# Kernel optimization log

Measured on AMD Instinct MI355X. Metric: run time of the kernel, lower is better.

Reference implementation:

```python
import jax, jax.numpy as jnp
import numpy as np

C, H, W = 8, 8, 8
A = 6            # action_dim
LATENT = 64
HID = 64
GRU_IN = HID + A + LATENT  # 134


def _conv(x, w):
    return jax.lax.conv_general_dilated(
        x, w, (1, 1), 'VALID', dimension_numbers=('NCHW', 'OIHW', 'NCHW'))


def setup_inputs() -> dict:
    key = jax.random.key(0)
    ks = jax.random.split(key, 20)
    B, N, T = 64, 10, 128
    s_h = jax.random.normal(ks[0], (B, N, T, C, H, W), jnp.float32)
    a_h = jax.random.randint(ks[1], (B, N, T), 0, A).astype(jnp.int64)
    b_z = jax.random.normal(ks[2], (B, LATENT), jnp.float32)
    s = 0.05
    p = {
        'conv1_w': jax.random.normal(ks[3], (32, C, 3, 3)) * s,
        'conv1_b': jnp.zeros((32,)),
        'conv2_w': jax.random.normal(ks[4], (32, 32, 3, 3)) * s,
        'conv2_b': jnp.zeros((32,)),
        'fc_w': jax.random.normal(ks[5], (HID, 32 * 4 * 4)) * s,
        'fc_b': jnp.zeros((HID,)),
        'emb': jax.random.normal(ks[6], (A, A)) * s,
        'gru_wih': jax.random.normal(ks[7], (3 * HID, GRU_IN)) * s,
        'gru_whh': jax.random.normal(ks[8], (3 * HID, HID)) * s,
        'gru_bih': jnp.zeros((3 * HID,)),
        'gru_bhh': jnp.zeros((3 * HID,)),
        'mlp1_w': jax.random.normal(ks[9], (HID, HID)) * s,
        'mlp1_b': jnp.zeros((HID,)),
        'mlp2_w': jax.random.normal(ks[10], (A, HID)) * s,
        'mlp2_b': jnp.zeros((A,)),
    }
    return {'s_h': s_h, 'a_h': a_h, 'b_z': b_z, **p}


def reference(s_h, a_h, b_z, conv1_w, conv1_b, conv2_w, conv2_b, fc_w, fc_b,
              emb, gru_wih, gru_whh, gru_bih, gru_bhh,
              mlp1_w, mlp1_b, mlp2_w, mlp2_b):
    B, N = s_h.shape[0], s_h.shape[1]
    T = a_h.shape[2]
    BN = B * N

    # action mask, [B, N, T, 1]
    action_masks = (a_h != A - 1)[..., None].astype(jnp.float32)

    # --- state encoder on first frame only ---
    s0 = s_h[:, :, 0].reshape(BN, C, H, W)
    x = jax.nn.relu(_conv(s0, conv1_w) + conv1_b[:, None, None])
    x = jax.nn.relu(_conv(x, conv2_w) + conv2_b[:, None, None])
    x = x.reshape(BN, -1)                       # [BN, 512]
    state_emb = jax.nn.relu(x @ fc_w.T + fc_b)  # [BN, HID]

    bz = jnp.broadcast_to(b_z[:, None, :], (B, N, LATENT)).reshape(BN, LATENT)

    h0 = jnp.zeros((BN, HID), s_h.dtype)
    act0 = jnp.full((BN,), A - 1, jnp.int32)

    def step(carry, _):
        h, act = carry
        a_emb = emb[act]                                          # [BN, A]
        inp = jnp.concatenate([state_emb, a_emb, bz], axis=-1)    # [BN, GRU_IN]
        gx = inp @ gru_wih.T + gru_bih
        gh = h @ gru_whh.T + gru_bhh
        xr, xz, xn = jnp.split(gx, 3, axis=-1)
        hr, hz, hn = jnp.split(gh, 3, axis=-1)
        r = jax.nn.sigmoid(xr + hr)
        z = jax.nn.sigmoid(xz + hz)
        n = jnp.tanh(xn + r * hn)
        h_new = (1.0 - z) * n + z * h
        hid = jnp.tanh(h_new @ mlp1_w.T + mlp1_b)
        logits = hid @ mlp2_w.T + mlp2_b                          # [BN, A]
        next_act = jax.lax.stop_gradient(jnp.argmax(logits, axis=-1)).astype(jnp.int32)
        return (h_new, next_act), logits

    (_, _), logits_seq = jax.lax.scan(step, (h0, act0), None, length=T - 1)
    # logits_seq: [T-1, BN, A] -> [B, N, T-1, A]
    logits_all = jnp.transpose(logits_seq, (1, 0, 2)).reshape(B, N, T - 1, A)
    return logits_all, action_masks
```

## Files before the change

kernel.cpp:

```cpp
#include <hip/hip_runtime.h>

#define A_DIM 6
#define HID_D 64
#define LATENT_D 64
#define GRU_IN_D 134
#define T_STEPS 128
#define N_ENV 10
#define BN_TOT 640

typedef float f2 __attribute__((ext_vector_type(2)));

__device__ __forceinline__ float fast_sigmoid(float x) {
    return __builtin_amdgcn_rcpf(1.0f + __builtin_amdgcn_exp2f(-1.4426950408889634f * x));
}
__device__ __forceinline__ float fast_tanh(float x) {
    return 1.0f - 2.0f * __builtin_amdgcn_rcpf(1.0f + __builtin_amdgcn_exp2f(2.8853900817779268f * x));
}

template<int CTRL>
__device__ __forceinline__ float dppadd(float v) {
    int t = __builtin_amdgcn_update_dpp(0, __builtin_bit_cast(int, v), CTRL, 0xf, 0xf, true);
    return v + __builtin_bit_cast(float, t);
}
__device__ __forceinline__ float wave_reduce_add(float v) {
    v = dppadd<0x111>(v);
    v = dppadd<0x112>(v);
    v = dppadd<0x114>(v);
    v = dppadd<0x118>(v);
    v = dppadd<0x142>(v);
    v = dppadd<0x143>(v);
    return __builtin_bit_cast(float, __builtin_amdgcn_readlane(__builtin_bit_cast(int, v), 63));
}

__global__ __launch_bounds__(128, 1)
void policy_kernel(const float* __restrict__ s_h,
                   const int*   __restrict__ a_h,
                   const float* __restrict__ b_z,
                   const float* __restrict__ conv1_w, const float* __restrict__ conv1_b,
                   const float* __restrict__ conv2_w, const float* __restrict__ conv2_b,
                   const float* __restrict__ fc_w,    const float* __restrict__ fc_b,
                   const float* __restrict__ emb,
                   const float* __restrict__ gru_wih, const float* __restrict__ gru_whh,
                   const float* __restrict__ gru_bih, const float* __restrict__ gru_bhh,
                   const float* __restrict__ mlp1_w,  const float* __restrict__ mlp1_b,
                   const float* __restrict__ mlp2_w,  const float* __restrict__ mlp2_b,
                   float* __restrict__ logits_out, float* __restrict__ mask_out)
{
    __shared__ __align__(16) float s0[512];
    __shared__ __align__(16) float a1[1152];
    __shared__ __align__(16) float a2[512];
    __shared__ __align__(16) float pfc[128];
    __shared__ __align__(16) float semb[64];
    __shared__ __align__(16) float gxc[192];
    __shared__ __align__(16) float atab[6*192];
    __shared__ __align__(16) float hspec[6*64];
    __shared__ f2 lwn2[2048];
    __shared__ f2 lw12[2048];

    const int bn  = blockIdx.x;
    const int tid = threadIdx.x;
    const int j   = tid & 63;
    const int w   = tid >> 6;

    mask_out[bn * T_STEPS + tid] = (a_h[bn * T_STEPS + tid] != (A_DIM - 1)) ? 1.0f : 0.0f;

    {
        const float* src = s_h + (size_t)bn * T_STEPS * 512;
        #pragma unroll
        for (int i = 0; i < 4; ++i) s0[tid + i * 128] = src[tid + i * 128];
    }

    for (int i2 = tid; i2 < 2048; i2 += 128) {
        const int k2 = i2 >> 6, jj = i2 & 63;
        lwn2[i2] = *(const f2*)&gru_whh[(128 + jj) * 64 + 2 * k2];
        lw12[i2] = *(const f2*)&mlp1_w[(size_t)jj * 64 + 2 * k2];
    }
    __syncthreads();

    for (int i = tid; i < 1152; i += 128) {
        const int oc = i / 36, r = i % 36, oh = r / 6, ow = r % 6;
        float sum = conv1_b[oc];
        const float* wp = conv1_w + oc * 72;
        #pragma unroll
        for (int ic = 0; ic < 8; ++ic)
            #pragma unroll
            for (int kh = 0; kh < 3; ++kh)
                #pragma unroll
                for (int kw = 0; kw < 3; ++kw)
                    sum = fmaf(s0[ic * 64 + (oh + kh) * 8 + (ow + kw)],
                               wp[ic * 9 + kh * 3 + kw], sum);
        a1[i] = fmaxf(sum, 0.0f);
    }
    __syncthreads();

    for (int i = tid; i < 512; i += 128) {
        const int oc = i / 16, r = i % 16, oh = r / 4, ow = r % 4;
        float sum = conv2_b[oc];
        const float* wp = conv2_w + oc * 288;
        for (int ic = 0; ic < 32; ++ic)
            #pragma unroll
            for (int kh = 0; kh < 3; ++kh)
                #pragma unroll
                for (int kw = 0; kw < 3; ++kw)
                    sum = fmaf(a1[ic * 36 + (oh + kh) * 6 + (ow + kw)],
                               wp[ic * 9 + kh * 3 + kw], sum);
        a2[i] = fmaxf(sum, 0.0f);
    }
    __syncthreads();

    {
        const float* wp = fc_w + j * 512 + w * 256;
        const float* ap = a2 + w * 256;
        float s0a = 0.f, s1a = 0.f, s2a = 0.f, s3a = 0.f;
        for (int k = 0; k < 256; k += 4) {
            s0a = fmaf(ap[k + 0], wp[k + 0], s0a);
            s1a = fmaf(ap[k + 1], wp[k + 1], s1a);
            s2a = fmaf(ap[k + 2], wp[k + 2], s2a);
            s3a = fmaf(ap[k + 3], wp[k + 3], s3a);
        }
        pfc[tid] = (s0a + s1a) + (s2a + s3a);
    }
    __syncthreads();
    if (tid < 64) semb[tid] = fmaxf(pfc[tid] + pfc[tid + 64] + fc_b[tid], 0.0f);
    __syncthreads();

    {
        const float* bz = b_z + (size_t)(bn / N_ENV) * LATENT_D;
        for (int g = tid; g < 192; g += 128) {
            float sum = gru_bih[g] + ((g < 128) ? gru_bhh[g] : 0.0f);
            const float* wp = gru_wih + g * GRU_IN_D;
            for (int k = 0; k < 64; ++k) sum = fmaf(semb[k], wp[k], sum);
            for (int k = 0; k < 64; ++k) sum = fmaf(bz[k], wp[70 + k], sum);
            gxc[g] = sum;
        }
    }
    for (int i = tid; i < 6 * 192; i += 128) {
        const int a = i / 192, g = i % 192;
        float sum = 0.0f;
        #pragma unroll
        for (int q = 0; q < 6; ++q)
            sum = fmaf(emb[a * 6 + q], gru_wih[g * GRU_IN_D + 64 + q], sum);
        atab[i] = sum;
    }
    __syncthreads();

    if (w == 1) return;

    f2 wr[32], wz[32];
    {
        const float* pr = gru_whh + (size_t)j * 64;
        const float* pz = gru_whh + (size_t)(64 + j) * 64;
        #pragma unroll
        for (int i = 0; i < 16; ++i) {
            float4 v;
            v = ((const float4*)pr)[i]; wr[2*i] = (f2){v.x, v.y}; wr[2*i+1] = (f2){v.z, v.w};
            v = ((const float4*)pz)[i]; wz[2*i] = (f2){v.x, v.y}; wz[2*i+1] = (f2){v.z, v.w};
        }
    }
    const float bhn = gru_bhh[128 + j];
    const float b1j = mlp1_b[j];
    float arx[6], azx[6], anx[6], m2c[6], b2[6];
    {
        const float gxr = gxc[j], gxz = gxc[64 + j], gxn = gxc[128 + j];
        #pragma unroll
        for (int a = 0; a < 6; ++a) {
            arx[a] = gxr + atab[a * 192 + j];
            azx[a] = gxz + atab[a * 192 + 64 + j];
            anx[a] = gxn + atab[a * 192 + 128 + j];
            m2c[a] = mlp2_w[a * 64 + j];
            b2[a] = mlp2_b[a];
        }
    }

    const f2* __restrict__ wnj = lwn2 + j;
    const f2* __restrict__ w1j = lw12 + j;

    float ha[6];
    #pragma unroll
    for (int a = 0; a < 6; ++a) {
        const float r = fast_sigmoid(arx[a]);
        const float z = fast_sigmoid(azx[a]);
        const float n = fast_tanh(fmaf(r, bhn, anx[a]));
        ha[a] = fmaf(z, 0.0f - n, n);
    }
    __builtin_amdgcn_wave_barrier();
    #pragma unroll
    for (int a = 0; a < 6; ++a) hspec[a * 64 + j] = ha[a];
    __builtin_amdgcn_wave_barrier();

    int act = A_DIM - 1;
    float* lout = logits_out + (size_t)bn * (T_STEPS - 1) * A_DIM;

    for (int t = 0; t < T_STEPS - 1; ++t) {
        const float4* hb = (const float4*)(hspec + (act << 6));
        float hprev = ha[0];
        #pragma unroll
        for (int a = 1; a < 6; ++a) hprev = (act == a) ? ha[a] : hprev;

        f2 p1a = {0.f, 0.f}, p1b = {0.f, 0.f};
        f2 pra = {0.f, 0.f}, prb = {0.f, 0.f};
        f2 pza = {0.f, 0.f}, pzb = {0.f, 0.f};
        f2 pna = {0.f, 0.f}, pnb = {0.f, 0.f};
        #pragma unroll
        for (int i = 0; i < 16; ++i) {
            const float4 hv = hb[i];
            const f2 hA = (f2){hv.x, hv.y};
            const f2 hB = (f2){hv.z, hv.w};
            pra += hA * wr[2*i];          prb += hB * wr[2*i+1];
            pza += hA * wz[2*i];          pzb += hB * wz[2*i+1];
            pna += hA * wnj[(2*i) * 64];  pnb += hB * wnj[(2*i+1) * 64];
            p1a += hA * w1j[(2*i) * 64];  p1b += hB * w1j[(2*i+1) * 64];
        }
        const f2 p1 = p1a + p1b;
        const float hid = fast_tanh(p1.x + p1.y + b1j);
        const f2 prf = pra + prb;
        const f2 pzf = pza + pzb;
        const f2 pnf = pna + pnb;
        const float hr = prf.x + prf.y;
        const float hz = pzf.x + pzf.y;
        const float hn = pnf.x + pnf.y + bhn;

        const float l0 = wave_reduce_add(hid * m2c[0]) + b2[0];
        const float l1 = wave_reduce_add(hid * m2c[1]) + b2[1];
        const float l2 = wave_reduce_add(hid * m2c[2]) + b2[2];
        const float l3 = wave_reduce_add(hid * m2c[3]) + b2[3];
        const float l4 = wave_reduce_add(hid * m2c[4]) + b2[4];
        const float l5 = wave_reduce_add(hid * m2c[5]) + b2[5];

        #pragma unroll
        for (int a = 0; a < 6; ++a) {
            const float r = fast_sigmoid(arx[a] + hr);
            const float z = fast_sigmoid(azx[a] + hz);
            const float n = fast_tanh(fmaf(r, hn, anx[a]));
            ha[a] = fmaf(z, hprev - n, n);
        }
        __builtin_amdgcn_wave_barrier();
        #pragma unroll
        for (int a = 0; a < 6; ++a) hspec[a * 64 + j] = ha[a];
        __builtin_amdgcn_wave_barrier();

        float best = l0; int bi = 0;
        if (l1 > best) { best = l1; bi = 1; }
        if (l2 > best) { best = l2; bi = 2; }
        if (l3 > best) { best = l3; bi = 3; }
        if (l4 > best) { best = l4; bi = 4; }
        if (l5 > best) { best = l5; bi = 5; }
        act = bi;

        if (j < A_DIM) {
            const float outv = (j == 0) ? l0 : (j == 1) ? l1 : (j == 2) ? l2
                             : (j == 3) ? l3 : (j == 4) ? l4 : l5;
            lout[t * A_DIM + j] = outv;
        }
    }
}

extern "C" void kernel_launch(void* const* d_in, const int* in_sizes, int n_in,
                              void* d_out, int out_size, void* d_ws, size_t ws_size,
                              hipStream_t stream) {
    const float* s_h     = (const float*)d_in[0];
    const int*   a_h     = (const int*)  d_in[1];
    const float* b_z     = (const float*)d_in[2];
    const float* conv1_w = (const float*)d_in[3];
    const float* conv1_b = (const float*)d_in[4];
    const float* conv2_w = (const float*)d_in[5];
    const float* conv2_b = (const float*)d_in[6];
    const float* fc_w    = (const float*)d_in[7];
    const float* fc_b    = (const float*)d_in[8];
    const float* emb     = (const float*)d_in[9];
    const float* gru_wih = (const float*)d_in[10];
    const float* gru_whh = (const float*)d_in[11];
    const float* gru_bih = (const float*)d_in[12];
    const float* gru_bhh = (const float*)d_in[13];
    const float* mlp1_w  = (const float*)d_in[14];
    const float* mlp1_b  = (const float*)d_in[15];
    const float* mlp2_w  = (const float*)d_in[16];
    const float* mlp2_b  = (const float*)d_in[17];

    float* out = (float*)d_out;
    float* logits_out = out;
    float* mask_out   = out + (size_t)BN_TOT * (T_STEPS - 1) * A_DIM;

    policy_kernel<<<BN_TOT, 128, 0, stream>>>(
        s_h, a_h, b_z, conv1_w, conv1_b, conv2_w, conv2_b, fc_w, fc_b, emb,
        gru_wih, gru_whh, gru_bih, gru_bhh, mlp1_w, mlp1_b, mlp2_w, mlp2_b,
        logits_out, mask_out);
}
```

Measured before the change: 490.0 us.

## Process two sequences per block with one wave interleaving both recurrences

Each block now handles two batch elements with 256 threads. The prologue runs in parallel per element, but a single wave runs both GRU recurrences interleaved, sharing the register and LDS weights. The action-embedding table is computed directly in registers instead of through shared memory. The aim is to hide latency on the serial per-step chain by giving the recurrence wave two independent dependency chains, and to halve the grid size. The cost is roughly double the per-step work on one wave, more register pressure, and half as many concurrently active recurrence waves (320 instead of 640).

```diff
diff --git a/kernel.cpp b/kernel.cpp
--- a/kernel.cpp
+++ b/kernel.cpp
@@ -7,6 +7,7 @@
 #define T_STEPS 128
 #define N_ENV 10
 #define BN_TOT 640
+#define NB 2
 
 typedef float f2 __attribute__((ext_vector_type(2)));
 
@@ -32,7 +33,7 @@
     return __builtin_bit_cast(float, __builtin_amdgcn_readlane(__builtin_bit_cast(int, v), 63));
 }
 
-__global__ __launch_bounds__(128, 1)
+__global__ __launch_bounds__(256, 2)
 void policy_kernel(const float* __restrict__ s_h,
                    const int*   __restrict__ a_h,
                    const float* __restrict__ b_z,
@@ -46,38 +47,40 @@
                    const float* __restrict__ mlp2_w,  const float* __restrict__ mlp2_b,
                    float* __restrict__ logits_out, float* __restrict__ mask_out)
 {
-    __shared__ __align__(16) float s0[512];
-    __shared__ __align__(16) float a1[1152];
-    __shared__ __align__(16) float a2[512];
-    __shared__ __align__(16) float pfc[128];
-    __shared__ __align__(16) float semb[64];
-    __shared__ __align__(16) float gxc[192];
-    __shared__ __align__(16) float atab[6*192];
-    __shared__ __align__(16) float hspec[6*64];
+    __shared__ __align__(16) float s0[NB][512];
+    __shared__ __align__(16) float a1[NB][1152];
+    __shared__ __align__(16) float a2[NB][512];
+    __shared__ __align__(16) float pfc[NB][128];
+    __shared__ __align__(16) float semb[NB][64];
+    __shared__ __align__(16) float gxc[NB][192];
+    __shared__ __align__(16) float hspec[NB][6*64];
     __shared__ f2 lwn2[2048];
     __shared__ f2 lw12[2048];
 
-    const int bn  = blockIdx.x;
-    const int tid = threadIdx.x;
-    const int j   = tid & 63;
-    const int w   = tid >> 6;
-
-    mask_out[bn * T_STEPS + tid] = (a_h[bn * T_STEPS + tid] != (A_DIM - 1)) ? 1.0f : 0.0f;
+    const int bn0  = blockIdx.x * NB;
+    const int tid  = threadIdx.x;
+    const int b    = tid >> 7;
+    const int ltid = tid & 127;
+    const int j    = tid & 63;
+    const int w    = (tid >> 6) & 1;
+    const int bn   = bn0 + b;
+
+    mask_out[bn * T_STEPS + ltid] = (a_h[bn * T_STEPS + ltid] != (A_DIM - 1)) ? 1.0f : 0.0f;
 
     {
         const float* src = s_h + (size_t)bn * T_STEPS * 512;
         #pragma unroll
-        for (int i = 0; i < 4; ++i) s0[tid + i * 128] = src[tid + i * 128];
-    }
-
-    for (int i2 = tid; i2 < 2048; i2 += 128) {
+        for (int i = 0; i < 4; ++i) s0[b][ltid + i * 128] = src[ltid + i * 128];
+    }
+
+    for (int i2 = tid; i2 < 2048; i2 += 256) {
         const int k2 = i2 >> 6, jj = i2 & 63;
         lwn2[i2] = *(const f2*)&gru_whh[(128 + jj) * 64 + 2 * k2];
         lw12[i2] = *(const f2*)&mlp1_w[(size_t)jj * 64 + 2 * k2];
     }
     __syncthreads();
 
-    for (int i = tid; i < 1152; i += 128) {
+    for (int i = ltid; i < 1152; i += 128) {
         const int oc = i / 36, r = i % 36, oh = r / 6, ow = r % 6;
         float sum = conv1_b[oc];
         const float* wp = conv1_w + oc * 72;
@@ -87,13 +90,13 @@
             for (int kh = 0; kh < 3; ++kh)
                 #pragma unroll
                 for (int kw = 0; kw < 3; ++kw)
-                    sum = fmaf(s0[ic * 64 + (oh + kh) * 8 + (ow + kw)],
+                    sum = fmaf(s0[b][ic * 64 + (oh + kh) * 8 + (ow + kw)],
                                wp[ic * 9 + kh * 3 + kw], sum);
-        a1[i] = fmaxf(sum, 0.0f);
-    }
-    __syncthreads();
-
-    for (int i = tid; i < 512; i += 128) {
+        a1[b][i] = fmaxf(sum, 0.0f);
+    }
+    __syncthreads();
+
+    for (int i = ltid; i < 512; i += 128) {
         const int oc = i / 16, r = i % 16, oh = r / 4, ow = r % 4;
         float sum = conv2_b[oc];
         const float* wp = conv2_w + oc * 288;
@@ -102,15 +105,15 @@
             for (int kh = 0; kh < 3; ++kh)
                 #pragma unroll
                 for (int kw = 0; kw < 3; ++kw)
-                    sum = fmaf(a1[ic * 36 + (oh + kh) * 6 + (ow + kw)],
+                    sum = fmaf(a1[b][ic * 36 + (oh + kh) * 6 + (ow + kw)],
                                wp[ic * 9 + kh * 3 + kw], sum);
-        a2[i] = fmaxf(sum, 0.0f);
+        a2[b][i] = fmaxf(sum, 0.0f);
     }
     __syncthreads();
 
     {
         const float* wp = fc_w + j * 512 + w * 256;
-        const float* ap = a2 + w * 256;
+        const float* ap = a2[b] + w * 256;
         float s0a = 0.f, s1a = 0.f, s2a = 0.f, s3a = 0.f;
         for (int k = 0; k < 256; k += 4) {
             s0a = fmaf(ap[k + 0], wp[k + 0], s0a);
@@ -118,33 +121,25 @@
             s2a = fmaf(ap[k + 2], wp[k + 2], s2a);
             s3a = fmaf(ap[k + 3], wp[k + 3], s3a);
         }
-        pfc[tid] = (s0a + s1a) + (s2a + s3a);
-    }
-    __syncthreads();
-    if (tid < 64) semb[tid] = fmaxf(pfc[tid] + pfc[tid + 64] + fc_b[tid], 0.0f);
+        pfc[b][ltid] = (s0a + s1a) + (s2a + s3a);
+    }
+    __syncthreads();
+    if (ltid < 64) semb[b][ltid] = fmaxf(pfc[b][ltid] + pfc[b][ltid + 64] + fc_b[ltid], 0.0f);
     __syncthreads();
 
     {
         const float* bz = b_z + (size_t)(bn / N_ENV) * LATENT_D;
-        for (int g = tid; g < 192; g += 128) {
+        for (int g = ltid; g < 192; g += 128) {
             float sum = gru_bih[g] + ((g < 128) ? gru_bhh[g] : 0.0f);
             const float* wp = gru_wih + g * GRU_IN_D;
-            for (int k = 0; k < 64; ++k) sum = fmaf(semb[k], wp[k], sum);
+            for (int k = 0; k < 64; ++k) sum = fmaf(semb[b][k], wp[k], sum);
             for (int k = 0; k < 64; ++k) sum = fmaf(bz[k], wp[70 + k], sum);
-            gxc[g] = sum;
-        }
-    }
-    for (int i = tid; i < 6 * 192; i += 128) {
-        const int a = i / 192, g = i % 192;
-        float sum = 0.0f;
-        #pragma unroll
-        for (int q = 0; q < 6; ++q)
-            sum = fmaf(emb[a * 6 + q], gru_wih[g * GRU_IN_D + 64 + q], sum);
-        atab[i] = sum;
-    }
-    __syncthreads();
-
-    if (w == 1) return;
+            gxc[b][g] = sum;
+        }
+    }
+    __syncthreads();
+
+    if (tid >= 64) return;
 
     f2 wr[32], wz[32];
     {
@@ -159,98 +154,151 @@
     }
     const float bhn = gru_bhh[128 + j];
     const float b1j = mlp1_b[j];
-    float arx[6], azx[6], anx[6], m2c[6], b2[6];
-    {
-        const float gxr = gxc[j], gxz = gxc[64 + j], gxn = gxc[128 + j];
+    float m2c[6], b2v[6];
+    #pragma unroll
+    for (int a = 0; a < 6; ++a) { m2c[a] = mlp2_w[a * 64 + j]; b2v[a] = mlp2_b[a]; }
+
+    float arx0[6], azx0[6], anx0[6], arx1[6], azx1[6], anx1[6];
+    {
+        float wqr[6], wqz[6], wqn[6];
+        #pragma unroll
+        for (int q = 0; q < 6; ++q) {
+            wqr[q] = gru_wih[j * GRU_IN_D + 64 + q];
+            wqz[q] = gru_wih[(64 + j) * GRU_IN_D + 64 + q];
+            wqn[q] = gru_wih[(128 + j) * GRU_IN_D + 64 + q];
+        }
+        const float g0r = gxc[0][j], g0z = gxc[0][64 + j], g0n = gxc[0][128 + j];
+        const float g1r = gxc[1][j], g1z = gxc[1][64 + j], g1n = gxc[1][128 + j];
         #pragma unroll
         for (int a = 0; a < 6; ++a) {
-            arx[a] = gxr + atab[a * 192 + j];
-            azx[a] = gxz + atab[a * 192 + 64 + j];
-            anx[a] = gxn + atab[a * 192 + 128 + j];
-            m2c[a] = mlp2_w[a * 64 + j];
-            b2[a] = mlp2_b[a];
+            float sr = 0.f, sz = 0.f, sn = 0.f;
+            #pragma unroll
+            for (int q = 0; q < 6; ++q) {
+                const float e = emb[a * 6 + q];
+                sr = fmaf(e, wqr[q], sr);
+                sz = fmaf(e, wqz[q], sz);
+                sn = fmaf(e, wqn[q], sn);
+            }
+            arx0[a] = g0r + sr; azx0[a] = g0z + sz; anx0[a] = g0n + sn;
+            arx1[a] = g1r + sr; azx1[a] = g1z + sz; anx1[a] = g1n + sn;
         }
     }
 
     const f2* __restrict__ wnj = lwn2 + j;
     const f2* __restrict__ w1j = lw12 + j;
 
-    float ha[6];
+    float ha0[6], ha1[6];
     #pragma unroll
     for (int a = 0; a < 6; ++a) {
-        const float r = fast_sigmoid(arx[a]);
-        const float z = fast_sigmoid(azx[a]);
-        const float n = fast_tanh(fmaf(r, bhn, anx[a]));
-        ha[a] = fmaf(z, 0.0f - n, n);
+        float r = fast_sigmoid(arx0[a]);
+        float z = fast_sigmoid(azx0[a]);
+        float n = fast_tanh(fmaf(r, bhn, anx0[a]));
+        ha0[a] = fmaf(z, 0.0f - n, n);
+        r = fast_sigmoid(arx1[a]);
+        z = fast_sigmoid(azx1[a]);
+        n = fast_tanh(fmaf(r, bhn, anx1[a]));
+        ha1[a] = fmaf(z, 0.0f - n, n);
     }
     __builtin_amdgcn_wave_barrier();
     #pragma unroll
-    for (int a = 0; a < 6; ++a) hspec[a * 64 + j] = ha[a];
+    for (int a = 0; a < 6; ++a) {
+        hspec[0][a * 64 + j] = ha0[a];
+        hspec[1][a * 64 + j] = ha1[a];
+    }
     __builtin_amdgcn_wave_barrier();
 
-    int act = A_DIM - 1;
-    float* lout = logits_out + (size_t)bn * (T_STEPS - 1) * A_DIM;
+    int act0 = A_DIM - 1, act1 = A_DIM - 1;
+    float* lo0 = logits_out + (size_t)(bn0 + 0) * (T_STEPS - 1) * A_DIM;
+    float* lo1 = logits_out + (size_t)(bn0 + 1) * (T_STEPS - 1) * A_DIM;
 
     for (int t = 0; t < T_STEPS - 1; ++t) {
-        const float4* hb = (const float4*)(hspec + (act << 6));
-        float hprev = ha[0];
-        #pragma unroll
-        for (int a = 1; a < 6; ++a) hprev = (act == a) ? ha[a] : hprev;
-
-        f2 p1a = {0.f, 0.f}, p1b = {0.f, 0.f};
-        f2 pra = {0.f, 0.f}, prb = {0.f, 0.f};
-        f2 pza = {0.f, 0.f}, pzb = {0.f, 0.f};
-        f2 pna = {0.f, 0.f}, pnb = {0.f, 0.f};
+        const float4* hbA = (const float4*)(hspec[0] + (act0 << 6));
+        const float4* hbB = (const float4*)(hspec[1] + (act1 << 6));
+        float hp0 = ha0[0], hp1 = ha1[0];
+        #pragma unroll
+        for (int a = 1; a < 6; ++a) {
+            hp0 = (act0 == a) ? ha0[a] : hp0;
+            hp1 = (act1 == a) ? ha1[a] : hp1;
+        }
+
+        f2 pr0 = {0.f,0.f}, pz0 = {0.f,0.f}, pn0 = {0.f,0.f}, p10 = {0.f,0.f};
+        f2 pr1 = {0.f,0.f}, pz1 = {0.f,0.f}, pn1 = {0.f,0.f}, p11 = {0.f,0.f};
         #pragma unroll
         for (int i = 0; i < 16; ++i) {
-            const float4 hv = hb[i];
-            const f2 hA = (f2){hv.x, hv.y};
-            const f2 hB = (f2){hv.z, hv.w};
-            pra += hA * wr[2*i];          prb += hB * wr[2*i+1];
-            pza += hA * wz[2*i];          pzb += hB * wz[2*i+1];
-            pna += hA * wnj[(2*i) * 64];  pnb += hB * wnj[(2*i+1) * 64];
-            p1a += hA * w1j[(2*i) * 64];  p1b += hB * w1j[(2*i+1) * 64];
-        }
-        const f2 p1 = p1a + p1b;
-        const float hid = fast_tanh(p1.x + p1.y + b1j);
-        const f2 prf = pra + prb;
-        const f2 pzf = pza + pzb;
-        const f2 pnf = pna + pnb;
-        const float hr = prf.x + prf.y;
-        const float hz = pzf.x + pzf.y;
-        const float hn = pnf.x + pnf.y + bhn;
-
-        const float l0 = wave_reduce_add(hid * m2c[0]) + b2[0];
-        const float l1 = wave_reduce_add(hid * m2c[1]) + b2[1];
-        const float l2 = wave_reduce_add(hid * m2c[2]) + b2[2];
-        const float l3 = wave_reduce_add(hid * m2c[3]) + b2[3];
-        const float l4 = wave_reduce_add(hid * m2c[4]) + b2[4];
-        const float l5 = wave_reduce_add(hid * m2c[5]) + b2[5];
+            const float4 hv0 = hbA[i];
+            const float4 hv1 = hbB[i];
+            const f2 h0A = (f2){hv0.x, hv0.y}, h0B = (f2){hv0.z, hv0.w};
+            const f2 h1A = (f2){hv1.x, hv1.y}, h1B = (f2){hv1.z, hv1.w};
+            const f2 wnA = wnj[(2*i) * 64], wnB = wnj[(2*i+1) * 64];
+            const f2 w1A = w1j[(2*i) * 64], w1B = w1j[(2*i+1) * 64];
+            pr0 += h0A * wr[2*i]; pr0 += h0B * wr[2*i+1];
+            pr1 += h1A * wr[2*i]; pr1 += h1B * wr[2*i+1];
+            pz0 += h0A * wz[2*i]; pz0 += h0B * wz[2*i+1];
+            pz1 += h1A * wz[2*i]; pz1 += h1B * wz[2*i+1];
+            pn0 += h0A * wnA;     pn0 += h0B * wnB;
+            pn1 += h1A * wnA;     pn1 += h1B * wnB;
+            p10 += h0A * w1A;     p10 += h0B * w1B;
+            p11 += h1A * w1A;     p11 += h1B * w1B;
+        }
+        const float hid0 = fast_tanh(p10.x + p10.y + b1j);
+        const float hid1 = fast_tanh(p11.x + p11.y + b1j);
+        const float hr0 = pr0.x + pr0.y, hz0 = pz0.x + pz0.y, hn0 = pn0.x + pn0.y + bhn;
+        const float hr1 = pr1.x + pr1.y, hz1 = pz1.x + pz1.y, hn1 = pn1.x + pn1.y + bhn;
+
+        const float l00 = wave_reduce_add(hid0 * m2c[0]) + b2v[0];
+        const float l01 = wave_reduce_add(hid0 * m2c[1]) + b2v[1];
+        const float l02 = wave_reduce_add(hid0 * m2c[2]) + b2v[2];
+        const float l03 = wave_reduce_add(hid0 * m2c[3]) + b2v[3];
+        const float l04 = wave_reduce_add(hid0 * m2c[4]) + b2v[4];
+        const float l05 = wave_reduce_add(hid0 * m2c[5]) + b2v[5];
+        const float l10 = wave_reduce_add(hid1 * m2c[0]) + b2v[0];
+        const float l11 = wave_reduce_add(hid1 * m2c[1]) + b2v[1];
+        const float l12 = wave_reduce_add(hid1 * m2c[2]) + b2v[2];
+        const float l13 = wave_reduce_add(hid1 * m2c[3]) + b2v[3];
+        const float l14 = wave_reduce_add(hid1 * m2c[4]) + b2v[4];
+        const float l15 = wave_reduce_add(hid1 * m2c[5]) + b2v[5];
 
         #pragma unroll
         for (int a = 0; a < 6; ++a) {
-            const float r = fast_sigmoid(arx[a] + hr);
-            const float z = fast_sigmoid(azx[a] + hz);
-            const float n = fast_tanh(fmaf(r, hn, anx[a]));
-            ha[a] = fmaf(z, hprev - n, n);
+            float r = fast_sigmoid(arx0[a] + hr0);
+            float z = fast_sigmoid(azx0[a] + hz0);
+            float n = fast_tanh(fmaf(r, hn0, anx0[a]));
+            ha0[a] = fmaf(z, hp0 - n, n);
+            r = fast_sigmoid(arx1[a] + hr1);
+            z = fast_sigmoid(azx1[a] + hz1);
+            n = fast_tanh(fmaf(r, hn1, anx1[a]));
+            ha1[a] = fmaf(z, hp1 - n, n);
         }
         __builtin_amdgcn_wave_barrier();
         #pragma unroll
-        for (int a = 0; a < 6; ++a) hspec[a * 64 + j] = ha[a];
+        for (int a = 0; a < 6; ++a) {
+            hspec[0][a * 64 + j] = ha0[a];
+            hspec[1][a * 64 + j] = ha1[a];
+        }
         __builtin_amdgcn_wave_barrier();
 
-        float best = l0; int bi = 0;
-        if (l1 > best) { best = l1; bi = 1; }
-        if (l2 > best) { best = l2; bi = 2; }
-        if (l3 > best) { best = l3; bi = 3; }
-        if (l4 > best) { best = l4; bi = 4; }
-        if (l5 > best) { best = l5; bi = 5; }
-        act = bi;
+        float best0 = l00; int bi0 = 0;
+        if (l01 > best0) { best0 = l01; bi0 = 1; }
+        if (l02 > best0) { best0 = l02; bi0 = 2; }
+        if (l03 > best0) { best0 = l03; bi0 = 3; }
+        if (l04 > best0) { best0 = l04; bi0 = 4; }
+        if (l05 > best0) { best0 = l05; bi0 = 5; }
+        act0 = bi0;
+        float best1 = l10; int bi1 = 0;
+        if (l11 > best1) { best1 = l11; bi1 = 1; }
+        if (l12 > best1) { best1 = l12; bi1 = 2; }
+        if (l13 > best1) { best1 = l13; bi1 = 3; }
+        if (l14 > best1) { best1 = l14; bi1 = 4; }
+        if (l15 > best1) { best1 = l15; bi1 = 5; }
+        act1 = bi1;
 
         if (j < A_DIM) {
-            const float outv = (j == 0) ? l0 : (j == 1) ? l1 : (j == 2) ? l2
-                             : (j == 3) ? l3 : (j == 4) ? l4 : l5;
-            lout[t * A_DIM + j] = outv;
+            const float o0 = (j == 0) ? l00 : (j == 1) ? l01 : (j == 2) ? l02
+                           : (j == 3) ? l03 : (j == 4) ? l04 : l05;
+            const float o1 = (j == 0) ? l10 : (j == 1) ? l11 : (j == 2) ? l12
+                           : (j == 3) ? l13 : (j == 4) ? l14 : l15;
+            lo0[t * A_DIM + j] = o0;
+            lo1[t * A_DIM + j] = o1;
         }
     }
 }
@@ -281,7 +329,7 @@
     float* logits_out = out;
     float* mask_out   = out + (size_t)BN_TOT * (T_STEPS - 1) * A_DIM;
 
-    policy_kernel<<<BN_TOT, 128, 0, stream>>>(
+    policy_kernel<<<BN_TOT / NB, 256, 0, stream>>>(
         s_h, a_h, b_z, conv1_w, conv1_b, conv2_w, conv2_b, fc_w, fc_b, emb,
         gru_wih, gru_whh, gru_bih, gru_bhh, mlp1_w, mlp1_b, mlp2_w, mlp2_b,
         logits_out, mask_out);
```

Result: slower. 576.4 us (+17.6%).
